# Kernel optimization log

Measured on AMD Instinct MI355X. Metric: run time of the kernel, lower is better.

## Reference

```python
import jax, jax.numpy as jnp
import numpy as np

GRID_SIZE = 16          # number of spline intervals; G+1 = 17 control points
KH, KW = 3, 3           # kernel size
EPS = 1e-8


def _extract_patches(x, kh, kw):
    """x: (B,H,W,C) -> patches (B,Ho,Wo,C,kh,kw), valid padding, stride 1."""
    B, H, W, C = x.shape
    Ho, Wo = H - kh + 1, W - kw + 1
    rows = []
    for i in range(kh):
        cols = []
        for j in range(kw):
            cols.append(x[:, i:i + Ho, j:j + Wo, :])  # (B,Ho,Wo,C)
        rows.append(jnp.stack(cols, axis=-1))          # (B,Ho,Wo,C,kw)
    return jnp.stack(rows, axis=-2)                    # (B,Ho,Wo,C,kh,kw)


def setup_inputs() -> dict:
    key = jax.random.key(0)
    k1, k2, k3, k4 = jax.random.split(key, 4)
    B, H, W, C, F = 4, 66, 66, 32, 64
    x = jax.random.normal(k1, (B, H, W, C), dtype=jnp.float32)
    control_points = jax.random.normal(k2, (F, C, KH, KW, GRID_SIZE + 1), dtype=jnp.float32) * 0.1
    w_spline = jax.random.normal(k3, (F, C, KH, KW), dtype=jnp.float32) * 0.1
    w_silu = jax.random.normal(k4, (F, C, KH, KW), dtype=jnp.float32) * 0.1
    bias = jnp.zeros((F,), dtype=jnp.float32)
    return {"x": x, "control_points": control_points, "w_spline": w_spline,
            "w_silu": w_silu, "bias": bias}


def reference(x, control_points, w_spline, w_silu, bias):
    # Fixed B-spline grid in [-1, 1]
    grid = jnp.linspace(-1.0, 1.0, GRID_SIZE + 1, dtype=x.dtype)  # (G+1,)
    grid_spacing = 2.0 / GRID_SIZE

    # Patch extraction (valid padding, stride 1)
    patches = _extract_patches(x, KH, KW)  # (B,Ho,Wo,C,kh,kw)

    # Linear B-spline (hat) basis with normalization
    xc = jnp.clip(patches, -1.0, 1.0)
    dist = jnp.abs(xc[..., None] - grid)                     # (B,Ho,Wo,C,kh,kw,G+1)
    w = jnp.maximum(0.0, 1.0 - dist / grid_spacing)
    basis = w / (jnp.sum(w, axis=-1, keepdims=True) + EPS)

    # K(x) = w_spline * spline(x) + w_silu * SiLU(x); reduce over (C,kh,kw) per filter
    cp_eff = w_spline[..., None] * control_points            # (F,C,kh,kw,G+1)
    spline_term = jnp.einsum('bhwcijg,fcijg->bhwf', basis, cp_eff)
    silu_term = jnp.einsum('bhwcij,fcij->bhwf', jax.nn.silu(patches), w_silu)

    return spline_term + silu_term + bias  # (B,Ho,Wo,F)
```

## Files before the change

kernel.cpp:

```cpp
#include <hip/hip_runtime.h>
#include <stdint.h>

typedef _Float16 half8 __attribute__((ext_vector_type(8)));
typedef float f32x16 __attribute__((ext_vector_type(16)));

#define NPX  (4 * 66 * 66 * 32)
#define NTH  (3 * 64 * 1728)
#define TH_OFF_BYTES ((size_t)NPX * 18 * 2)
#define PREP_BLOCKS  ((NPX + NTH) / 256)

__global__ __launch_bounds__(256) void kan_prep(
    const float* __restrict__ x, const float* __restrict__ cp,
    const float* __restrict__ wspl, const float* __restrict__ wsil,
    _Float16* __restrict__ Ff, _Float16* __restrict__ th)
{
    int tid = blockIdx.x * 256 + threadIdx.x;
    if (tid < NPX) {
        float p  = x[tid];
        float xc = fminf(1.0f, fmaxf(-1.0f, p));
        float u  = fmaf(xc, 8.0f, 8.0f);
        union { _Float16 h[18]; uint32_t w[9]; } pk;
#pragma unroll
        for (int m = 0; m < 17; ++m)
            pk.h[m] = (_Float16)fmaxf(0.0f, 1.0f - fabsf(u - (float)m));
        pk.h[17] = (_Float16)(p * __builtin_amdgcn_rcpf(1.0f + __expf(-p)));
        uint32_t* dst = (uint32_t*)(Ff + (size_t)tid * 18);
#pragma unroll
        for (int q = 0; q < 9; ++q) dst[q] = pk.w[q];
    } else if (tid < NPX + NTH) {
        int e  = tid - NPX;
        int k  = e % 1728;
        int fi = e / 1728;
        int f  = fi & 63;
        int i  = fi >> 6;
        int j  = k / 576;
        int q  = k - j * 576;
        int c  = q / 18;
        int m  = q - c * 18;
        int base = ((f * 32 + c) * 3 + i) * 3 + j;
        float v = (m < 17) ? wspl[base] * cp[base * 17 + m] : wsil[base];
        th[e] = (_Float16)v;
    }
}

__global__ __launch_bounds__(256) void kan_main(
    const _Float16* __restrict__ Ff, const _Float16* __restrict__ th,
    const float* __restrict__ bias, float* __restrict__ out)
{
    __shared__ _Float16 lA[2][64 * 72];
    __shared__ _Float16 lB[2][64 * 72];

    const int bx = blockIdx.x;
    const int i  = blockIdx.y;
    const int b  = bx >> 6;
    const int ho = bx & 63;

    const int tid  = threadIdx.x;
    const int wv   = tid >> 6;
    const int wpx  = wv >> 1;
    const int wf   = wv & 1;
    const int lane = tid & 63;
    const int r31  = lane & 31;
    const int kh   = lane >> 5;

    const int srow = tid >> 2;
    const int sq   = tid & 3;

    const _Float16* gA = Ff
        + ((size_t)((b * 66 + ho + i) * 66 + srow)) * 576 + sq * 16;
    const _Float16* gB = th
        + ((size_t)(i * 64 + srow)) * 1728 + sq * 16;

    uint4 pA0, pA1, pB0, pB1;
#define LOADCH(ch)                                                \
    {                                                             \
        const uint4* qa = (const uint4*)(gA + (ch) * 64);         \
        pA0 = qa[0]; pA1 = qa[1];                                 \
        const uint4* qb = (const uint4*)(gB + (ch) * 64);         \
        pB0 = qb[0]; pB1 = qb[1];                                 \
    }

    LOADCH(0)

    f32x16 acc;
    {
        float bv = (i == 1) ? bias[wf * 32 + r31] : 0.0f;
#pragma unroll
        for (int r = 0; r < 16; ++r) acc[r] = bv;
    }

    const int aoff = (wpx * 32 + r31) * 72 + kh * 8;
    const int boff = (wf  * 32 + r31) * 72 + kh * 8;
    char* wbA = (char*)lA[0] + srow * 144 + sq * 32;
    char* wbB = (char*)lB[0] + srow * 144 + sq * 32;

    int cur = 0;
    for (int ch = 0; ch < 27; ++ch) {
        uint4* dA = (uint4*)(wbA + cur * 9216);
        uint4* dB = (uint4*)(wbB + cur * 9216);
        dA[0] = pA0; dA[1] = pA1;
        dB[0] = pB0; dB[1] = pB1;
        __syncthreads();
        if (ch < 26) LOADCH(ch + 1)
        const _Float16* pa = lA[cur] + aoff;
        const _Float16* pb = lB[cur] + boff;
#pragma unroll
        for (int s = 0; s < 4; ++s) {
            half8 a  = *(const half8*)(pa + s * 16);
            half8 bf = *(const half8*)(pb + s * 16);
            acc = __builtin_amdgcn_mfma_f32_32x32x16_f16(a, bf, acc, 0, 0, 0);
        }
        cur ^= 1;
    }
#undef LOADCH

    float* obase = out
        + ((size_t)((b * 64 + ho) * 64 + wpx * 32)) * 64 + wf * 32;
#pragma unroll
    for (int r = 0; r < 16; ++r) {
        int rowD = (r & 3) + 8 * (r >> 2) + 4 * kh;
        atomicAdd(obase + (size_t)rowD * 64 + r31, acc[r]);
    }
}

extern "C" void kernel_launch(void* const* d_in, const int* in_sizes, int n_in,
                              void* d_out, int out_size, void* d_ws, size_t ws_size,
                              hipStream_t stream) {
    const float* x    = (const float*)d_in[0];
    const float* cp   = (const float*)d_in[1];
    const float* wspl = (const float*)d_in[2];
    const float* wsil = (const float*)d_in[3];
    const float* bias = (const float*)d_in[4];
    float* out = (float*)d_out;

    uint8_t* ws = (uint8_t*)d_ws;
    _Float16* Ff = (_Float16*)ws;
    _Float16* th = (_Float16*)(ws + TH_OFF_BYTES);

    kan_prep<<<PREP_BLOCKS, 256, 0, stream>>>(x, cp, wspl, wsil, Ff, th);
    hipMemsetAsync(d_out, 0, (size_t)out_size * 4, stream);

    dim3 grid(256, 3);
    kan_main<<<grid, 256, 0, stream>>>(Ff, th, bias, out);
}
```

Baseline: 106.3 us.

## Build sparse hat-basis A tiles in LDS from x inside the main kernel

Drops the precomputed 18-wide fp16 basis buffer. The main kernel now reads raw x and writes the two nonzero hat-basis weights plus the SiLU value straight into a zeroed shared-memory A tile, clearing the previous nonzeros each chunk. Chunks become 144 wide (12 chunks, 9 MFMAs each) with single-buffered LDS and two barriers per chunk. This removes a large global write and read of the expanded basis, at the cost of less load/compute overlap and scattered 2-byte LDS stores.

Result: slower. 119.4 us (+12.3%).

```diff
diff --git a/kernel.cpp b/kernel.cpp
--- a/kernel.cpp
+++ b/kernel.cpp
@@ -4,51 +4,33 @@
 typedef _Float16 half8 __attribute__((ext_vector_type(8)));
 typedef float f32x16 __attribute__((ext_vector_type(16)));
 
-#define NPX  (4 * 66 * 66 * 32)
 #define NTH  (3 * 64 * 1728)
-#define TH_OFF_BYTES ((size_t)NPX * 18 * 2)
-#define PREP_BLOCKS  ((NPX + NTH) / 256)
+#define PREP_BLOCKS (NTH / 256)
 
 __global__ __launch_bounds__(256) void kan_prep(
-    const float* __restrict__ x, const float* __restrict__ cp,
-    const float* __restrict__ wspl, const float* __restrict__ wsil,
-    _Float16* __restrict__ Ff, _Float16* __restrict__ th)
+    const float* __restrict__ cp, const float* __restrict__ wspl,
+    const float* __restrict__ wsil, _Float16* __restrict__ th)
 {
-    int tid = blockIdx.x * 256 + threadIdx.x;
-    if (tid < NPX) {
-        float p  = x[tid];
-        float xc = fminf(1.0f, fmaxf(-1.0f, p));
-        float u  = fmaf(xc, 8.0f, 8.0f);
-        union { _Float16 h[18]; uint32_t w[9]; } pk;
-#pragma unroll
-        for (int m = 0; m < 17; ++m)
-            pk.h[m] = (_Float16)fmaxf(0.0f, 1.0f - fabsf(u - (float)m));
-        pk.h[17] = (_Float16)(p * __builtin_amdgcn_rcpf(1.0f + __expf(-p)));
-        uint32_t* dst = (uint32_t*)(Ff + (size_t)tid * 18);
-#pragma unroll
-        for (int q = 0; q < 9; ++q) dst[q] = pk.w[q];
-    } else if (tid < NPX + NTH) {
-        int e  = tid - NPX;
-        int k  = e % 1728;
-        int fi = e / 1728;
-        int f  = fi & 63;
-        int i  = fi >> 6;
-        int j  = k / 576;
-        int q  = k - j * 576;
-        int c  = q / 18;
-        int m  = q - c * 18;
-        int base = ((f * 32 + c) * 3 + i) * 3 + j;
-        float v = (m < 17) ? wspl[base] * cp[base * 17 + m] : wsil[base];
-        th[e] = (_Float16)v;
-    }
+    int e  = blockIdx.x * 256 + threadIdx.x;
+    int k  = e % 1728;
+    int fi = e / 1728;
+    int f  = fi & 63;
+    int i  = fi >> 6;
+    int j  = k / 576;
+    int q  = k - j * 576;
+    int c  = q / 18;
+    int m  = q - c * 18;
+    int base = ((f * 32 + c) * 3 + i) * 3 + j;
+    float v = (m < 17) ? wspl[base] * cp[base * 17 + m] : wsil[base];
+    th[e] = (_Float16)v;
 }
 
 __global__ __launch_bounds__(256) void kan_main(
-    const _Float16* __restrict__ Ff, const _Float16* __restrict__ th,
+    const float* __restrict__ x, const _Float16* __restrict__ th,
     const float* __restrict__ bias, float* __restrict__ out)
 {
-    __shared__ _Float16 lA[2][64 * 72];
-    __shared__ _Float16 lB[2][64 * 72];
+    __shared__ __align__(16) _Float16 lA[64 * 152];
+    __shared__ __align__(16) _Float16 lB[64 * 152];
 
     const int bx = blockIdx.x;
     const int i  = blockIdx.y;
@@ -63,24 +45,36 @@
     const int r31  = lane & 31;
     const int kh   = lane >> 5;
 
-    const int srow = tid >> 2;
-    const int sq   = tid & 3;
+    int goffB[5], doffB[5];
+#pragma unroll
+    for (int r = 0; r < 5; ++r) {
+        int id  = tid + 256 * r;
+        int row = id / 18;
+        int u   = id - row * 18;
+        goffB[r] = row * 3456 + u * 16;
+        doffB[r] = row * 304 + u * 16;
+    }
+    const char* thb = (const char*)(th + (size_t)(i * 64) * 1728);
 
-    const _Float16* gA = Ff
-        + ((size_t)((b * 66 + ho + i) * 66 + srow)) * 576 + sq * 16;
-    const _Float16* gB = th
-        + ((size_t)(i * 64 + srow)) * 1728 + sq * 16;
+    const int apx = tid >> 2;
+    const int cc  = tid & 3;
+    const float* xrow = x + ((size_t)((b * 66 + ho + i) * 66 + apx)) * 32;
+    char* aBase = (char*)lA + apx * 304 + cc * 72;
+    char* pprev0 = aBase + 30;
+    char* pprev1 = aBase + 36 + 30;
 
-    uint4 pA0, pA1, pB0, pB1;
-#define LOADCH(ch)                                                \
-    {                                                             \
-        const uint4* qa = (const uint4*)(gA + (ch) * 64);         \
-        pA0 = qa[0]; pA1 = qa[1];                                 \
-        const uint4* qb = (const uint4*)(gB + (ch) * 64);         \
-        pB0 = qb[0]; pB1 = qb[1];                                 \
+    for (int o = tid * 8; o < 64 * 304; o += 2048)
+        *(uint64_t*)((char*)lA + o) = 0ull;
+
+    uint4 bPF[5];
+    float2 xPF;
+    {
+#pragma unroll
+        for (int r = 0; r < 5; ++r)
+            if (r < 4 || tid < 128)
+                bPF[r] = *(const uint4*)(thb + goffB[r]);
+        xPF = *(const float2*)(xrow + cc * 2);
     }
-
-    LOADCH(0)
 
     f32x16 acc;
     {
@@ -89,30 +83,70 @@
         for (int r = 0; r < 16; ++r) acc[r] = bv;
     }
 
-    const int aoff = (wpx * 32 + r31) * 72 + kh * 8;
-    const int boff = (wf  * 32 + r31) * 72 + kh * 8;
-    char* wbA = (char*)lA[0] + srow * 144 + sq * 32;
-    char* wbB = (char*)lB[0] + srow * 144 + sq * 32;
+    const _Float16* pa = lA + (wpx * 32 + r31) * 152 + kh * 8;
+    const _Float16* pb = lB + (wf  * 32 + r31) * 152 + kh * 8;
 
-    int cur = 0;
-    for (int ch = 0; ch < 27; ++ch) {
-        uint4* dA = (uint4*)(wbA + cur * 9216);
-        uint4* dB = (uint4*)(wbB + cur * 9216);
-        dA[0] = pA0; dA[1] = pA1;
-        dB[0] = pB0; dB[1] = pB1;
+    __syncthreads();
+
+#pragma unroll
+    for (int ch = 0; ch < 12; ++ch) {
+        const int jn = ch >> 2, octn = ch & 3;
+#pragma unroll
+        for (int r = 0; r < 5; ++r)
+            if (r < 4 || tid < 128)
+                *(uint4*)((char*)lB + doffB[r]) = bPF[r];
+        if (ch < 11) {
+            const int j2 = (ch + 1) >> 2, o2 = (ch + 1) & 3;
+            const int kb2 = j2 * 1152 + o2 * 288;
+#pragma unroll
+            for (int r = 0; r < 5; ++r)
+                if (r < 4 || tid < 128)
+                    bPF[r] = *(const uint4*)(thb + goffB[r] + kb2);
+        }
+        {
+            float p0 = xPF.x, p1 = xPF.y;
+            *(_Float16*)(pprev0) = (_Float16)0.0f;
+            *(_Float16*)(pprev0 + 2) = (_Float16)0.0f;
+            *(_Float16*)(pprev1) = (_Float16)0.0f;
+            *(_Float16*)(pprev1 + 2) = (_Float16)0.0f;
+            {
+                float xc = fminf(1.0f, fmaxf(-1.0f, p0));
+                float u  = fmaf(xc, 8.0f, 8.0f);
+                int  f0  = min((int)u, 15);
+                float fr = u - (float)f0;
+                char* ad = aBase + f0 * 2;
+                *(_Float16*)(ad)     = (_Float16)(1.0f - fr);
+                *(_Float16*)(ad + 2) = (_Float16)fr;
+                *(_Float16*)(aBase + 34) =
+                    (_Float16)(p0 * __builtin_amdgcn_rcpf(1.0f + __expf(-p0)));
+                pprev0 = ad;
+            }
+            {
+                float xc = fminf(1.0f, fmaxf(-1.0f, p1));
+                float u  = fmaf(xc, 8.0f, 8.0f);
+                int  f0  = min((int)u, 15);
+                float fr = u - (float)f0;
+                char* ad = aBase + 36 + f0 * 2;
+                *(_Float16*)(ad)     = (_Float16)(1.0f - fr);
+                *(_Float16*)(ad + 2) = (_Float16)fr;
+                *(_Float16*)(aBase + 36 + 34) =
+                    (_Float16)(p1 * __builtin_amdgcn_rcpf(1.0f + __expf(-p1)));
+                pprev1 = ad;
+            }
+        }
+        if (ch < 11) {
+            const int j2 = (ch + 1) >> 2, o2 = (ch + 1) & 3;
+            xPF = *(const float2*)(xrow + j2 * 32 + o2 * 8 + cc * 2);
+        }
         __syncthreads();
-        if (ch < 26) LOADCH(ch + 1)
-        const _Float16* pa = lA[cur] + aoff;
-        const _Float16* pb = lB[cur] + boff;
 #pragma unroll
-        for (int s = 0; s < 4; ++s) {
+        for (int s = 0; s < 9; ++s) {
             half8 a  = *(const half8*)(pa + s * 16);
             half8 bf = *(const half8*)(pb + s * 16);
             acc = __builtin_amdgcn_mfma_f32_32x32x16_f16(a, bf, acc, 0, 0, 0);
         }
-        cur ^= 1;
+        if (ch < 11) __syncthreads();
     }
-#undef LOADCH
 
     float* obase = out
         + ((size_t)((b * 64 + ho) * 64 + wpx * 32)) * 64 + wf * 32;
@@ -133,13 +167,11 @@
     const float* bias = (const float*)d_in[4];
     float* out = (float*)d_out;
 
-    uint8_t* ws = (uint8_t*)d_ws;
-    _Float16* Ff = (_Float16*)ws;
-    _Float16* th = (_Float16*)(ws + TH_OFF_BYTES);
+    _Float16* th = (_Float16*)d_ws;
 
-    kan_prep<<<PREP_BLOCKS, 256, 0, stream>>>(x, cp, wspl, wsil, Ff, th);
+    kan_prep<<<PREP_BLOCKS, 256, 0, stream>>>(cp, wspl, wsil, th);
     hipMemsetAsync(d_out, 0, (size_t)out_size * 4, stream);
 
     dim3 grid(256, 3);
-    kan_main<<<grid, 256, 0, stream>>>(Ff, th, bias, out);
+    kan_main<<<grid, 256, 0, stream>>>(x, th, bias, out);
 }
```
